# Kernel tuning notes

Measured on AMD Instinct MI355X. Metric: run time of the kernel, lower is better.

## Reference

```python
import jax, jax.numpy as jnp
import numpy as np


def setup_inputs() -> dict:
    key = jax.random.key(0)
    k1, k2, k3 = jax.random.split(key, 3)
    N = 20000
    # valid [x1, y1, x2, y2] boxes: centers in [0,1000), sizes in [1,101)
    xy = jax.random.uniform(k1, (N, 2), dtype=jnp.float32) * 1000.0
    wh = jax.random.uniform(k2, (N, 2), dtype=jnp.float32) * 100.0 + 1.0
    boxes = jnp.concatenate([xy, xy + wh], axis=1)
    scores = jax.random.uniform(k3, (N,), dtype=jnp.float32)
    return {
        "boxes": boxes,
        "scores": scores,
        "max_output_size": 1000,
        "iou_threshold": 0.5,
        "scores_threshold": 0.1,
    }


def reference(boxes, scores, max_output_size, iou_threshold, scores_threshold):
    boxes = boxes.astype(jnp.float32)
    scores = scores.astype(jnp.float32)
    N = boxes.shape[0]

    # score filtering: instead of physically filtering (dynamic shape),
    # mark below-threshold boxes as pre-suppressed and push them to the
    # end of the stable descending sort with -inf keys.
    valid = scores > scores_threshold
    sort_key = jnp.where(valid, scores, -jnp.inf)
    order = jnp.argsort(-sort_key)  # jnp.argsort is stable -> stable descending

    sboxes = boxes[order]                      # [N,4] score-sorted boxes
    svalid = valid[order]
    sorig = order.astype(jnp.int32)            # original indices, sorted
    areas = (sboxes[:, 2] - sboxes[:, 0]) * (sboxes[:, 3] - sboxes[:, 1])
    idx = jnp.arange(N)

    def body(carry, i):
        suppressed, selected, count = carry
        can = jnp.logical_and(~suppressed[i], count < max_output_size)
        selected = jnp.where(can, selected.at[count].set(sorig[i]), selected)
        # vectorized IoU of box i against all boxes (only j > i matter)
        b = sboxes[i]
        x1 = jnp.maximum(b[0], sboxes[:, 0])
        y1 = jnp.maximum(b[1], sboxes[:, 1])
        x2 = jnp.minimum(b[2], sboxes[:, 2])
        y2 = jnp.minimum(b[3], sboxes[:, 3])
        inter = jnp.maximum(x2 - x1, 0.0) * jnp.maximum(y2 - y1, 0.0)
        union = jnp.maximum(areas[i] + areas - inter, 1e-6)
        iou = inter / union
        suppressed = suppressed | (can & (idx > i) & (iou >= iou_threshold))
        count = count + can.astype(jnp.int32)
        return (suppressed, selected, count), None

    init = (~svalid, jnp.zeros(max_output_size, dtype=jnp.int32), jnp.int32(0))
    (_, selected, count), _ = jax.lax.scan(body, init, idx)
    return selected, count
```

## Files before the change

### kernel.cpp

```cpp
#include <hip/hip_runtime.h>
#include <cstdint>

typedef unsigned long long u64;

#define TOPK 2048
#define MW2 (TOPK / 64)
#define CAND 4096
#define HIST_BLOCKS 8
#define COMPACT_BLOCKS 32
#define RANK_BLOCKS (CAND / 64)
#define FB_WORDS 1024


__device__ __forceinline__ unsigned score_ud(float s, float thr) {
    unsigned u = __float_as_uint(s);
    u ^= (u >> 31) ? 0xFFFFFFFFu : 0x80000000u;
    unsigned ud = ~u;
    if (!(s > thr)) ud = 0xFFFFFFFFu;
    return ud;
}

__global__ __launch_bounds__(256) void hist_kernel(const float* __restrict__ scores,
                                                   const float* __restrict__ thrPtr,
                                                   int* __restrict__ slices,
                                                   int* __restrict__ meta, int N) {
    __shared__ int h[4096];
    int tid = threadIdx.x;
    for (int b = tid; b < 4096; b += 256) h[b] = 0;
    if (blockIdx.x == 0 && tid == 0) meta[0] = 0;
    __syncthreads();
    float thr = *thrPtr;
    for (int i = blockIdx.x * 256 + tid; i < N; i += HIST_BLOCKS * 256) {
        unsigned ud = score_ud(scores[i], thr);
        if (ud != 0xFFFFFFFFu) atomicAdd(&h[ud >> 20], 1);
    }
    __syncthreads();
    int* myslice = slices + blockIdx.x * 4096;
    for (int b = tid; b < 4096; b += 256) myslice[b] = h[b];
}

__global__ __launch_bounds__(256) void compact_kernel(
        const float* __restrict__ scores, const float* __restrict__ thrPtr,
        const int* __restrict__ slices, int* __restrict__ meta,
        u64* __restrict__ ckeys, int N, int maxNeed) {
    __shared__ int bins[4096];
    __shared__ int shC;
    int tid = threadIdx.x, lane = tid & 63;
    {
        const int4* sl = (const int4*)slices;
        int4* bo = (int4*)bins;
#pragma unroll
        for (int k = 0; k < 4; ++k) {
            int p = k * 256 + tid;
            int4 a = sl[p];
            int4 v1 = sl[1024 + p];
            int4 v2 = sl[2 * 1024 + p];
            int4 v3 = sl[3 * 1024 + p];
            int4 v4 = sl[4 * 1024 + p];
            int4 v5 = sl[5 * 1024 + p];
            int4 v6 = sl[6 * 1024 + p];
            int4 v7 = sl[7 * 1024 + p];
            a.x += v1.x + v2.x + v3.x + v4.x + v5.x + v6.x + v7.x;
            a.y += v1.y + v2.y + v3.y + v4.y + v5.y + v6.y + v7.y;
            a.z += v1.z + v2.z + v3.z + v4.z + v5.z + v6.z + v7.z;
            a.w += v1.w + v2.w + v3.w + v4.w + v5.w + v6.w + v7.w;
            bo[p] = a;
        }
    }
    __syncthreads();
    if (tid < 64) {
        int base = lane * 64;
        int sum = 0;
        for (int b = 0; b < 64; ++b) sum += bins[base + ((b + lane) & 63)];
        int incl = sum;
        for (int off = 1; off < 64; off <<= 1) {
            int o = __shfl_up(incl, off, 64);
            if (lane >= off) incl += o;
        }
        int total = __shfl(incl, 63, 64);
        int need = (maxNeed < total) ? maxNeed : total;
        u64 ok = __ballot(incl >= need);
        int L = (ok != 0ull) ? (int)__builtin_ctzll(ok) : 0;
        if (lane == L) {
            int acc = incl - sum;
            int C = base, Msel = acc;
            for (int b = 0; b < 64; ++b) {
                acc += bins[base + b];
                if (acc >= need) { C = base + b; Msel = acc; break; }
            }
            if (need <= 0) { C = -1; Msel = 0; }
            shC = C;
            if (blockIdx.x == 0) {
                meta[2] = Msel;
                meta[3] = (Msel > CAND) ? 1 : 0;
            }
        }
        if (lane == 0 && blockIdx.x == 0) meta[1] = total;
    }
    __syncthreads();
    int C = shC;
    float thr = *thrPtr;
    for (int i0 = blockIdx.x * 256; i0 < N; i0 += COMPACT_BLOCKS * 256) {
        int i = i0 + tid;
        bool sel = false;
        unsigned ud = 0;
        if (i < N) {
            ud = score_ud(scores[i], thr);
            sel = (ud != 0xFFFFFFFFu) && ((int)(ud >> 20) <= C);
        }
        u64 ball = __ballot(sel);
        if (ball) {
            int cntw = __popcll(ball);
            int base = 0;
            if (lane == 0) base = atomicAdd(&meta[0], cntw);
            base = __shfl(base, 0, 64);
            if (sel) {
                int slot = base + __popcll(ball & ((1ull << lane) - 1ull));
                if (slot < CAND) ckeys[slot] = ((u64)ud << 32) | (unsigned)i;
            }
        }
    }
}

__global__ __launch_bounds__(256) void rank_gather_kernel(
        const u64* __restrict__ ckeys, const int* __restrict__ meta,
        const float* __restrict__ boxes,
        float4* __restrict__ sboxes, int* __restrict__ sorig) {
    __shared__ u64 lk[CAND];
    __shared__ int part[4][64];
    int tid = threadIdx.x, lane = tid & 63, q = tid >> 6;
    int Msel = meta[2];
    if (Msel > CAND) Msel = CAND;
    for (int j = tid; j < Msel; j += 256) lk[j] = ckeys[j];
    __syncthreads();
    if (blockIdx.x * 64 >= Msel) return;
    int i = blockIdx.x * 64 + lane;
    u64 key = (i < Msel) ? lk[i] : ~0ull;
    int chunk = (Msel + 3) >> 2;
    int j0 = q * chunk;
    int j1 = j0 + chunk; if (j1 > Msel) j1 = Msel;
    int r = 0;
#pragma unroll 4
    for (int j = j0; j < j1; ++j) r += (lk[j] < key) ? 1 : 0;
    part[q][lane] = r;
    __syncthreads();
    if (q == 0 && i < Msel) {
        int rank = part[0][lane] + part[1][lane] + part[2][lane] + part[3][lane];
        if (rank < TOPK) {
            int idx = (int)(key & 0xFFFFFFFFu);
            sboxes[rank] = ((const float4*)boxes)[idx];
            sorig[rank] = idx;
        }
    }
}

__global__ __launch_bounds__(64) void mask2_kernel(
        const float4* __restrict__ sboxes, const float* __restrict__ iouThrPtr,
        u64* __restrict__ maskT, u64* __restrict__ diagT) {
    int wi = blockIdx.x, wj = blockIdx.y;
    if (wj < wi) return;
    __shared__ float jx1[64], jy1[64], jx2[64], jy2[64], ja[64];
    __shared__ u64 rowLDS[64];
    int t = threadIdx.x;
    int j0 = wj << 6;
    float4 jb = sboxes[j0 + t];
    jx1[t] = jb.x; jy1[t] = jb.y; jx2[t] = jb.z; jy2[t] = jb.w;
    ja[t] = (jb.z - jb.x) * (jb.w - jb.y);
    __syncthreads();
    int i = (wi << 6) + t;
    float thr = *iouThrPtr;
    float4 ib = sboxes[i];
    float ia = (ib.z - ib.x) * (ib.w - ib.y);
    u64 bits = 0;
    for (int jj = 0; jj < 64; ++jj) {
        int j = j0 + jj;
        if (j > i) {
            float xx1 = fmaxf(ib.x, jx1[jj]);
            float yy1 = fmaxf(ib.y, jy1[jj]);
            float xx2 = fminf(ib.z, jx2[jj]);
            float yy2 = fminf(ib.w, jy2[jj]);
            float ww = fmaxf(xx2 - xx1, 0.0f);
            float hh = fmaxf(yy2 - yy1, 0.0f);
            float inter = ww * hh;
            float uni = fmaxf(ia + ja[jj] - inter, 1e-6f);
            if (inter / uni >= thr) bits |= 1ull << jj;
        }
    }
    rowLDS[t] = bits;
    __syncthreads();
    u64 col = 0;
    for (int r = 0; r < 64; ++r) col |= ((rowLDS[r] >> t) & 1ull) << r;
    maskT[(size_t)(j0 + t) * MW2 + wi] = col;
    if (wi == wj) diagT[(wi << 6) + t] = col;
}

__global__ __launch_bounds__(1024) void scan2_kernel(
        const u64* __restrict__ maskT, const u64* __restrict__ diagT,
        const int* __restrict__ sorig, const int* __restrict__ meta,
        const float* __restrict__ boxes, const float* __restrict__ scores,
        const float* __restrict__ iouThrPtr, const float* __restrict__ scoreThrPtr,
        int* __restrict__ out, int N, int maxOut) {
    __shared__ u64 diagLDS[TOPK];
    __shared__ u64 selw[MW2];
    __shared__ u64 validwLDS[MW2];
    __shared__ u64 ballots[4];
    __shared__ int selLDS[TOPK];
    __shared__ int cntSh;
    __shared__ u64 aliveW[FB_WORDS];
    __shared__ u64 keyRed[16];
    __shared__ u64 winKeySh;
    int tid = threadIdx.x, lane = tid & 63, wave = tid >> 6;

    int Msel = meta[2];
    int V = (Msel < TOPK) ? Msel : TOPK;
    for (int k = tid; k < TOPK; k += 1024) diagLDS[k] = diagT[k];
    if (tid < MW2) {
        int lo = tid * 64;
        u64 vw = (V >= lo + 64) ? ~0ull : ((V > lo) ? ((1ull << (V - lo)) - 1ull) : 0ull);
        validwLDS[tid] = vw;
        selw[tid] = 0ull;
    }
    if (tid == 0) cntSh = 0;

    ulonglong2 a0, a1, a2, a3;
    int cc = tid >> 2, g = tid & 3;
    if (tid < 256) {
        const ulonglong2* p = (const ulonglong2*)(maskT + (size_t)cc * MW2 + g * 8);
        a0 = p[0]; a1 = p[1]; a2 = p[2]; a3 = p[3];
    }
    __syncthreads();

    int cnt = 0;
    for (int w = 0; w < MW2; ++w) {
        if (tid < 256) {
            u64 wd0 = a0.x, wd1 = a0.y, wd2 = a1.x, wd3 = a1.y;
            u64 wd4 = a2.x, wd5 = a2.y, wd6 = a3.x, wd7 = a3.y;
            int wr0 = g * 8;
            u64 acc = 0;
            if (wr0 + 0 < w) acc |= wd0 & selw[wr0 + 0];
            if (wr0 + 1 < w) acc |= wd1 & selw[wr0 + 1];
            if (wr0 + 2 < w) acc |= wd2 & selw[wr0 + 2];
            if (wr0 + 3 < w) acc |= wd3 & selw[wr0 + 3];
            if (wr0 + 4 < w) acc |= wd4 & selw[wr0 + 4];
            if (wr0 + 5 < w) acc |= wd5 & selw[wr0 + 5];
            if (wr0 + 6 < w) acc |= wd6 & selw[wr0 + 6];
            if (wr0 + 7 < w) acc |= wd7 & selw[wr0 + 7];
            acc |= __shfl_xor(acc, 1, 64);
            acc |= __shfl_xor(acc, 2, 64);
            u64 B = __ballot(acc != 0ull);
            if (lane == 0) ballots[wave] = B;
            if (w + 1 < MW2) {
                const ulonglong2* p = (const ulonglong2*)(maskT + (size_t)((w + 1) * 64 + cc) * MW2 + g * 8);
                a0 = p[0]; a1 = p[1]; a2 = p[2]; a3 = p[3];
            }
        }
        __syncthreads();
        if (wave == 0) {
            u64 bv = ballots[lane >> 4];
            bool crossk = (bv >> ((lane & 15) << 2)) & 1ull;
            bool alv = ((validwLDS[w] >> lane) & 1ull) && !crossk;
            u64 inm = diagLDS[(w << 6) | lane];
            u64 sel = __ballot(alv);
            for (int it = 0; it < 64; ++it) {
                bool killed = (inm & sel) != 0ull;
                u64 ns = __ballot(alv && !killed);
                if (ns == sel) break;
                sel = ns;
            }
            int room = maxOut - cnt;
            int tot = __popcll(sel);
            u64 below = (1ull << lane) - 1ull;
            if (tot > room) {
                bool keep = ((sel >> lane) & 1ull) && (__popcll(sel & below) < room);
                sel = __ballot(keep);
                tot = room;
            }
            if ((sel >> lane) & 1ull) {
                int pos = cnt + __popcll(sel & below);
                selLDS[pos] = (w << 6) | lane;
            }
            if (lane == 0) { selw[w] = sel; cntSh = cnt + tot; }
        }
        __syncthreads();
        cnt = cntSh;
        if (cnt >= maxOut) break;
    }

    int vt = meta[1];
    int f2 = meta[3];
    bool complete = (f2 == 0) && ((cnt >= maxOut) || (V >= vt));
    if (complete) {
        for (int k = tid; k < cnt; k += 1024) out[k] = sorig[selLDS[k]];
        for (int k = cnt + tid; k < maxOut; k += 1024) out[k] = 0;
        if (tid == 0) out[maxOut] = cnt;
        return;
    }

    float sThr = *scoreThrPtr, iThr = *iouThrPtr;
    for (int e0 = wave << 6; e0 < N; e0 += 1024) {
        int e = e0 + lane;
        bool a = (e < N) && (scores[e] > sThr);
        u64 ball = __ballot(a);
        if (lane == 0) aliveW[e0 >> 6] = ball;
    }
    __syncthreads();
    int fcnt = 0;
    while (fcnt < maxOut) {
        u64 best = 0;
        for (int e = tid; e < N; e += 1024) {
            if ((aliveW[e >> 6] >> (e & 63)) & 1ull) {
                float s = scores[e];
                unsigned u = __float_as_uint(s);
                u ^= (u >> 31) ? 0xFFFFFFFFu : 0x80000000u;
                u64 k = ((u64)u << 32) | (unsigned)(~e);
                if (k > best) best = k;
            }
        }
#pragma unroll
        for (int off = 32; off >= 1; off >>= 1) {
            u64 o = __shfl_xor(best, off, 64);
            if (o > best) best = o;
        }
        if (lane == 0) keyRed[wave] = best;
        __syncthreads();
        if (tid == 0) {
            u64 b = 0;
            for (int p = 0; p < 16; ++p) if (keyRed[p] > b) b = keyRed[p];
            winKeySh = b;
        }
        __syncthreads();
        u64 wk = winKeySh;
        if (wk == 0ull) break;
        int win = (int)(~(unsigned)wk);
        if (tid == 0) out[fcnt] = win;
        ++fcnt;
        float4 wb = ((const float4*)boxes)[win];
        float wa = (wb.z - wb.x) * (wb.w - wb.y);
        for (int e0 = wave << 6; e0 < N; e0 += 1024) {
            int e = e0 + lane;
            bool kill = false;
            if (e < N && ((aliveW[e0 >> 6] >> lane) & 1ull)) {
                if (e == win) kill = true;
                else {
                    float4 bb = ((const float4*)boxes)[e];
                    float xx1 = fmaxf(wb.x, bb.x), yy1 = fmaxf(wb.y, bb.y);
                    float xx2 = fminf(wb.z, bb.z), yy2 = fminf(wb.w, bb.w);
                    float inter = fmaxf(xx2 - xx1, 0.0f) * fmaxf(yy2 - yy1, 0.0f);
                    float ba = (bb.z - bb.x) * (bb.w - bb.y);
                    float uni = fmaxf(wa + ba - inter, 1e-6f);
                    kill = (inter / uni >= iThr);
                }
            }
            u64 kb = __ballot(kill);
            if (lane == 0 && kb) aliveW[e0 >> 6] &= ~kb;
        }
        __syncthreads();
    }
    for (int k = fcnt + tid; k < maxOut; k += 1024) out[k] = 0;
    if (tid == 0) out[maxOut] = fcnt;
}

extern "C" void kernel_launch(void* const* d_in, const int* in_sizes, int n_in,
                              void* d_out, int out_size, void* d_ws, size_t ws_size,
                              hipStream_t stream) {
    const float* boxes       = (const float*)d_in[0];
    const float* scores      = (const float*)d_in[1];
    const float* iouThrPtr   = (const float*)d_in[3];
    const float* scoreThrPtr = (const float*)d_in[4];

    int N = in_sizes[0] / 4;
    int maxOut = out_size - 1;

    char* ws = (char*)d_ws;
    size_t off = 0;
    auto take = [&](size_t b) { void* p = ws + off; off = (off + b + 255) & ~(size_t)255; return p; };
    int*    slices = (int*)   take((size_t)HIST_BLOCKS * 4096 * 4);
    int*    meta   = (int*)   take(256);
    u64*    ckeys  = (u64*)   take((size_t)CAND * 8);
    float4* sboxes = (float4*)take((size_t)TOPK * 16);
    int*    sorig  = (int*)   take((size_t)TOPK * 4);
    u64*    maskT  = (u64*)   take((size_t)TOPK * MW2 * 8);
    u64*    diagT  = (u64*)   take((size_t)MW2 * 64 * 8);
    (void)ws_size;

    hist_kernel<<<HIST_BLOCKS, 256, 0, stream>>>(scores, scoreThrPtr, slices, meta, N);
    compact_kernel<<<COMPACT_BLOCKS, 256, 0, stream>>>(scores, scoreThrPtr, slices, meta,
                                                       ckeys, N, TOPK);
    rank_gather_kernel<<<RANK_BLOCKS, 256, 0, stream>>>(ckeys, meta, boxes, sboxes, sorig);
    mask2_kernel<<<dim3(MW2, MW2), 64, 0, stream>>>(sboxes, iouThrPtr, maskT, diagT);
    scan2_kernel<<<1, 1024, 0, stream>>>(maskT, diagT, sorig, meta,
                                         boxes, scores, iouThrPtr, scoreThrPtr,
                                         (int*)d_out, N, maxOut);
}
```

Before: 64.54 us.

## Fuse NMS pipeline into single cooperative kernel with grid syncs

Replaces the five separate kernel launches (histogram, compaction, rank/gather, mask build, scan) with one cooperative kernel of 256 blocks that separates the phases with grid.sync(). The aim is to remove launch gaps and inter-kernel dependency stalls. The mask phase now packs four 64-wide tiles per block over only the upper-triangular tiles, and the histogram uses 16 blocks. In exchange, the final sequential scan runs on one 256-thread block instead of 1024 threads, and cooperative grid-sync costs are added.

```diff
diff --git a/kernel.cpp b/kernel.cpp
--- a/kernel.cpp
+++ b/kernel.cpp
@@ -1,14 +1,16 @@
 #include <hip/hip_runtime.h>
+#include <hip/hip_cooperative_groups.h>
 #include <cstdint>
 
+namespace cg = cooperative_groups;
 typedef unsigned long long u64;
 
 #define TOPK 2048
 #define MW2 (TOPK / 64)
 #define CAND 4096
-#define HIST_BLOCKS 8
-#define COMPACT_BLOCKS 32
-#define RANK_BLOCKS (CAND / 64)
+#define NB 256
+#define NT 256
+#define HISTB 16
 #define FB_WORDS 1024
 
 
@@ -20,92 +22,109 @@
     return ud;
 }
 
-__global__ __launch_bounds__(256) void hist_kernel(const float* __restrict__ scores,
-                                                   const float* __restrict__ thrPtr,
-                                                   int* __restrict__ slices,
-                                                   int* __restrict__ meta, int N) {
-    __shared__ int h[4096];
-    int tid = threadIdx.x;
-    for (int b = tid; b < 4096; b += 256) h[b] = 0;
-    if (blockIdx.x == 0 && tid == 0) meta[0] = 0;
-    __syncthreads();
-    float thr = *thrPtr;
-    for (int i = blockIdx.x * 256 + tid; i < N; i += HIST_BLOCKS * 256) {
-        unsigned ud = score_ud(scores[i], thr);
-        if (ud != 0xFFFFFFFFu) atomicAdd(&h[ud >> 20], 1);
-    }
-    __syncthreads();
-    int* myslice = slices + blockIdx.x * 4096;
-    for (int b = tid; b < 4096; b += 256) myslice[b] = h[b];
-}
-
-__global__ __launch_bounds__(256) void compact_kernel(
-        const float* __restrict__ scores, const float* __restrict__ thrPtr,
-        const int* __restrict__ slices, int* __restrict__ meta,
-        u64* __restrict__ ckeys, int N, int maxNeed) {
-    __shared__ int bins[4096];
-    __shared__ int shC;
-    int tid = threadIdx.x, lane = tid & 63;
-    {
-        const int4* sl = (const int4*)slices;
-        int4* bo = (int4*)bins;
+struct SMem {
+    union {
+        int bins[4096];
+        u64 lk[CAND];
+        struct {
+            float jx1[4][64], jy1[4][64], jx2[4][64], jy2[4][64], ja[4][64];
+            u64 rowLDS[4][64];
+        } mk;
+        struct {
+            u64 diagLDS[TOPK];
+            int selLDS[TOPK];
+            u64 aliveW[FB_WORDS];
+        } sc;
+    } u;
+    int part[4][64];
+    u64 selw[MW2];
+    u64 validwLDS[MW2];
+    u64 ballots[4];
+    u64 keyRed[4];
+    u64 winKeySh;
+    int cntSh;
+};
+
+__global__ __launch_bounds__(NT) void nms_all_kernel(
+        const float* __restrict__ scores, const float* __restrict__ scoreThrPtr,
+        const float* __restrict__ boxes, const float* __restrict__ iouThrPtr,
+        int* __restrict__ slices, int* __restrict__ meta,
+        u64* __restrict__ ckeys, float4* __restrict__ sboxes,
+        int* __restrict__ sorig, u64* __restrict__ maskT, u64* __restrict__ diagT,
+        int* __restrict__ out, int N, int maxOut) {
+    __shared__ SMem sm;
+    cg::grid_group grid = cg::this_grid();
+    int tid = threadIdx.x, lane = tid & 63, wave = tid >> 6;
+    int bid = blockIdx.x;
+    float sThr = *scoreThrPtr;
+
+    if (bid < HISTB) {
+        for (int b = tid; b < 4096; b += NT) sm.u.bins[b] = 0;
+        __syncthreads();
+        for (int i = bid * NT + tid; i < N; i += HISTB * NT) {
+            unsigned ud = score_ud(scores[i], sThr);
+            if (ud != 0xFFFFFFFFu) atomicAdd(&sm.u.bins[ud >> 20], 1);
+        }
+        __syncthreads();
+        int* sl = slices + bid * 4096;
+        for (int b = tid; b < 4096; b += NT) sl[b] = sm.u.bins[b];
+    }
+    if (bid == 0 && tid == 0) meta[0] = 0;
+    grid.sync();
+
+    if (bid == 0) {
+        const int4* sl4 = (const int4*)slices;
+        int4* bo = (int4*)sm.u.bins;
 #pragma unroll
         for (int k = 0; k < 4; ++k) {
-            int p = k * 256 + tid;
-            int4 a = sl[p];
-            int4 v1 = sl[1024 + p];
-            int4 v2 = sl[2 * 1024 + p];
-            int4 v3 = sl[3 * 1024 + p];
-            int4 v4 = sl[4 * 1024 + p];
-            int4 v5 = sl[5 * 1024 + p];
-            int4 v6 = sl[6 * 1024 + p];
-            int4 v7 = sl[7 * 1024 + p];
-            a.x += v1.x + v2.x + v3.x + v4.x + v5.x + v6.x + v7.x;
-            a.y += v1.y + v2.y + v3.y + v4.y + v5.y + v6.y + v7.y;
-            a.z += v1.z + v2.z + v3.z + v4.z + v5.z + v6.z + v7.z;
-            a.w += v1.w + v2.w + v3.w + v4.w + v5.w + v6.w + v7.w;
-            bo[p] = a;
-        }
-    }
-    __syncthreads();
-    if (tid < 64) {
-        int base = lane * 64;
-        int sum = 0;
-        for (int b = 0; b < 64; ++b) sum += bins[base + ((b + lane) & 63)];
-        int incl = sum;
-        for (int off = 1; off < 64; off <<= 1) {
-            int o = __shfl_up(incl, off, 64);
-            if (lane >= off) incl += o;
-        }
-        int total = __shfl(incl, 63, 64);
-        int need = (maxNeed < total) ? maxNeed : total;
-        u64 ok = __ballot(incl >= need);
-        int L = (ok != 0ull) ? (int)__builtin_ctzll(ok) : 0;
-        if (lane == L) {
-            int acc = incl - sum;
-            int C = base, Msel = acc;
-            for (int b = 0; b < 64; ++b) {
-                acc += bins[base + b];
-                if (acc >= need) { C = base + b; Msel = acc; break; }
-            }
-            if (need <= 0) { C = -1; Msel = 0; }
-            shC = C;
-            if (blockIdx.x == 0) {
+            int p = k * NT + tid;
+            int ax = 0, ay = 0, az = 0, aw = 0;
+#pragma unroll
+            for (int s = 0; s < HISTB; ++s) {
+                int4 v = sl4[s * 1024 + p];
+                ax += v.x; ay += v.y; az += v.z; aw += v.w;
+            }
+            int4 o; o.x = ax; o.y = ay; o.z = az; o.w = aw;
+            bo[p] = o;
+        }
+        __syncthreads();
+        if (tid < 64) {
+            int base = lane * 64;
+            int sum = 0;
+            for (int b = 0; b < 64; ++b) sum += sm.u.bins[base + ((b + lane) & 63)];
+            int incl = sum;
+            for (int off = 1; off < 64; off <<= 1) {
+                int o = __shfl_up(incl, off, 64);
+                if (lane >= off) incl += o;
+            }
+            int total = __shfl(incl, 63, 64);
+            int need = (TOPK < total) ? TOPK : total;
+            u64 ok = __ballot(incl >= need);
+            int L = (ok != 0ull) ? (int)__builtin_ctzll(ok) : 0;
+            if (lane == L) {
+                int acc = incl - sum;
+                int C = base, Msel = acc;
+                for (int b = 0; b < 64; ++b) {
+                    acc += sm.u.bins[base + b];
+                    if (acc >= need) { C = base + b; Msel = acc; break; }
+                }
+                if (need <= 0) { C = -1; Msel = 0; }
                 meta[2] = Msel;
                 meta[3] = (Msel > CAND) ? 1 : 0;
-            }
-        }
-        if (lane == 0 && blockIdx.x == 0) meta[1] = total;
-    }
-    __syncthreads();
-    int C = shC;
-    float thr = *thrPtr;
-    for (int i0 = blockIdx.x * 256; i0 < N; i0 += COMPACT_BLOCKS * 256) {
-        int i = i0 + tid;
+                meta[4] = C;
+            }
+            if (lane == 0) meta[1] = total;
+        }
+    }
+    grid.sync();
+
+    {
+        int C = meta[4];
+        int i = bid * NT + tid;
         bool sel = false;
         unsigned ud = 0;
         if (i < N) {
-            ud = score_ud(scores[i], thr);
+            ud = score_ud(scores[i], sThr);
             sel = (ud != 0xFFFFFFFFu) && ((int)(ud >> 20) <= C);
         }
         u64 ball = __ballot(sel);
@@ -120,111 +139,102 @@
             }
         }
     }
-}
-
-__global__ __launch_bounds__(256) void rank_gather_kernel(
-        const u64* __restrict__ ckeys, const int* __restrict__ meta,
-        const float* __restrict__ boxes,
-        float4* __restrict__ sboxes, int* __restrict__ sorig) {
-    __shared__ u64 lk[CAND];
-    __shared__ int part[4][64];
-    int tid = threadIdx.x, lane = tid & 63, q = tid >> 6;
-    int Msel = meta[2];
-    if (Msel > CAND) Msel = CAND;
-    for (int j = tid; j < Msel; j += 256) lk[j] = ckeys[j];
-    __syncthreads();
-    if (blockIdx.x * 64 >= Msel) return;
-    int i = blockIdx.x * 64 + lane;
-    u64 key = (i < Msel) ? lk[i] : ~0ull;
-    int chunk = (Msel + 3) >> 2;
-    int j0 = q * chunk;
-    int j1 = j0 + chunk; if (j1 > Msel) j1 = Msel;
-    int r = 0;
+    grid.sync();
+
+    {
+        int Msel = meta[2];
+        if (Msel > CAND) Msel = CAND;
+        if (bid * 64 < Msel) {
+            for (int j = tid; j < Msel; j += NT) sm.u.lk[j] = ckeys[j];
+            __syncthreads();
+            int q = tid >> 6;
+            int i = bid * 64 + lane;
+            u64 key = (i < Msel) ? sm.u.lk[i] : ~0ull;
+            int chunk = (Msel + 3) >> 2;
+            int j0 = q * chunk;
+            int j1 = j0 + chunk; if (j1 > Msel) j1 = Msel;
+            int r = 0;
 #pragma unroll 4
-    for (int j = j0; j < j1; ++j) r += (lk[j] < key) ? 1 : 0;
-    part[q][lane] = r;
-    __syncthreads();
-    if (q == 0 && i < Msel) {
-        int rank = part[0][lane] + part[1][lane] + part[2][lane] + part[3][lane];
-        if (rank < TOPK) {
-            int idx = (int)(key & 0xFFFFFFFFu);
-            sboxes[rank] = ((const float4*)boxes)[idx];
-            sorig[rank] = idx;
-        }
-    }
-}
-
-__global__ __launch_bounds__(64) void mask2_kernel(
-        const float4* __restrict__ sboxes, const float* __restrict__ iouThrPtr,
-        u64* __restrict__ maskT, u64* __restrict__ diagT) {
-    int wi = blockIdx.x, wj = blockIdx.y;
-    if (wj < wi) return;
-    __shared__ float jx1[64], jy1[64], jx2[64], jy2[64], ja[64];
-    __shared__ u64 rowLDS[64];
-    int t = threadIdx.x;
-    int j0 = wj << 6;
-    float4 jb = sboxes[j0 + t];
-    jx1[t] = jb.x; jy1[t] = jb.y; jx2[t] = jb.z; jy2[t] = jb.w;
-    ja[t] = (jb.z - jb.x) * (jb.w - jb.y);
-    __syncthreads();
-    int i = (wi << 6) + t;
-    float thr = *iouThrPtr;
-    float4 ib = sboxes[i];
-    float ia = (ib.z - ib.x) * (ib.w - ib.y);
-    u64 bits = 0;
-    for (int jj = 0; jj < 64; ++jj) {
-        int j = j0 + jj;
-        if (j > i) {
-            float xx1 = fmaxf(ib.x, jx1[jj]);
-            float yy1 = fmaxf(ib.y, jy1[jj]);
-            float xx2 = fminf(ib.z, jx2[jj]);
-            float yy2 = fminf(ib.w, jy2[jj]);
-            float ww = fmaxf(xx2 - xx1, 0.0f);
-            float hh = fmaxf(yy2 - yy1, 0.0f);
-            float inter = ww * hh;
-            float uni = fmaxf(ia + ja[jj] - inter, 1e-6f);
-            if (inter / uni >= thr) bits |= 1ull << jj;
-        }
-    }
-    rowLDS[t] = bits;
-    __syncthreads();
-    u64 col = 0;
-    for (int r = 0; r < 64; ++r) col |= ((rowLDS[r] >> t) & 1ull) << r;
-    maskT[(size_t)(j0 + t) * MW2 + wi] = col;
-    if (wi == wj) diagT[(wi << 6) + t] = col;
-}
-
-__global__ __launch_bounds__(1024) void scan2_kernel(
-        const u64* __restrict__ maskT, const u64* __restrict__ diagT,
-        const int* __restrict__ sorig, const int* __restrict__ meta,
-        const float* __restrict__ boxes, const float* __restrict__ scores,
-        const float* __restrict__ iouThrPtr, const float* __restrict__ scoreThrPtr,
-        int* __restrict__ out, int N, int maxOut) {
-    __shared__ u64 diagLDS[TOPK];
-    __shared__ u64 selw[MW2];
-    __shared__ u64 validwLDS[MW2];
-    __shared__ u64 ballots[4];
-    __shared__ int selLDS[TOPK];
-    __shared__ int cntSh;
-    __shared__ u64 aliveW[FB_WORDS];
-    __shared__ u64 keyRed[16];
-    __shared__ u64 winKeySh;
-    int tid = threadIdx.x, lane = tid & 63, wave = tid >> 6;
+            for (int j = j0; j < j1; ++j) r += (sm.u.lk[j] < key) ? 1 : 0;
+            sm.part[q][lane] = r;
+            __syncthreads();
+            if (q == 0 && i < Msel) {
+                int rank = sm.part[0][lane] + sm.part[1][lane] +
+                           sm.part[2][lane] + sm.part[3][lane];
+                if (rank < TOPK) {
+                    int idx = (int)(key & 0xFFFFFFFFu);
+                    sboxes[rank] = ((const float4*)boxes)[idx];
+                    sorig[rank] = idx;
+                }
+            }
+        }
+    }
+    grid.sync();
+
+    {
+        float iThr = *iouThrPtr;
+        int g = tid >> 6;
+        int t = bid * 4 + g;
+        const int ntiles = (MW2 * (MW2 + 1)) / 2;
+        bool act = (t < ntiles);
+        int wi = 0, tt = t;
+        if (act) { while (tt >= MW2 - wi) { tt -= MW2 - wi; ++wi; } }
+        int wj = wi + tt;
+        if (act) {
+            float4 jb = sboxes[(wj << 6) + lane];
+            sm.u.mk.jx1[g][lane] = jb.x; sm.u.mk.jy1[g][lane] = jb.y;
+            sm.u.mk.jx2[g][lane] = jb.z; sm.u.mk.jy2[g][lane] = jb.w;
+            sm.u.mk.ja[g][lane] = (jb.z - jb.x) * (jb.w - jb.y);
+        }
+        __syncthreads();
+        u64 bits = 0;
+        if (act) {
+            int i = (wi << 6) + lane;
+            float4 ib = sboxes[i];
+            float ia = (ib.z - ib.x) * (ib.w - ib.y);
+            int j0 = wj << 6;
+            for (int jj = 0; jj < 64; ++jj) {
+                int j = j0 + jj;
+                if (j > i) {
+                    float xx1 = fmaxf(ib.x, sm.u.mk.jx1[g][jj]);
+                    float yy1 = fmaxf(ib.y, sm.u.mk.jy1[g][jj]);
+                    float xx2 = fminf(ib.z, sm.u.mk.jx2[g][jj]);
+                    float yy2 = fminf(ib.w, sm.u.mk.jy2[g][jj]);
+                    float ww = fmaxf(xx2 - xx1, 0.0f);
+                    float hh = fmaxf(yy2 - yy1, 0.0f);
+                    float inter = ww * hh;
+                    float uni = fmaxf(ia + sm.u.mk.ja[g][jj] - inter, 1e-6f);
+                    if (inter / uni >= iThr) bits |= 1ull << jj;
+                }
+            }
+            sm.u.mk.rowLDS[g][lane] = bits;
+        }
+        __syncthreads();
+        if (act) {
+            u64 col = 0;
+            for (int r = 0; r < 64; ++r) col |= ((sm.u.mk.rowLDS[g][r] >> lane) & 1ull) << r;
+            maskT[(size_t)((wj << 6) + lane) * MW2 + wi] = col;
+            if (wi == wj) diagT[(wi << 6) + lane] = col;
+        }
+    }
+    grid.sync();
+
+    if (bid != 0) return;
 
     int Msel = meta[2];
     int V = (Msel < TOPK) ? Msel : TOPK;
-    for (int k = tid; k < TOPK; k += 1024) diagLDS[k] = diagT[k];
+    for (int k = tid; k < TOPK; k += NT) sm.u.sc.diagLDS[k] = diagT[k];
     if (tid < MW2) {
         int lo = tid * 64;
         u64 vw = (V >= lo + 64) ? ~0ull : ((V > lo) ? ((1ull << (V - lo)) - 1ull) : 0ull);
-        validwLDS[tid] = vw;
-        selw[tid] = 0ull;
-    }
-    if (tid == 0) cntSh = 0;
+        sm.validwLDS[tid] = vw;
+        sm.selw[tid] = 0ull;
+    }
+    if (tid == 0) sm.cntSh = 0;
 
     ulonglong2 a0, a1, a2, a3;
     int cc = tid >> 2, g = tid & 3;
-    if (tid < 256) {
+    {
         const ulonglong2* p = (const ulonglong2*)(maskT + (size_t)cc * MW2 + g * 8);
         a0 = p[0]; a1 = p[1]; a2 = p[2]; a3 = p[3];
     }
@@ -232,23 +242,23 @@
 
     int cnt = 0;
     for (int w = 0; w < MW2; ++w) {
-        if (tid < 256) {
+        {
             u64 wd0 = a0.x, wd1 = a0.y, wd2 = a1.x, wd3 = a1.y;
             u64 wd4 = a2.x, wd5 = a2.y, wd6 = a3.x, wd7 = a3.y;
             int wr0 = g * 8;
             u64 acc = 0;
-            if (wr0 + 0 < w) acc |= wd0 & selw[wr0 + 0];
-            if (wr0 + 1 < w) acc |= wd1 & selw[wr0 + 1];
-            if (wr0 + 2 < w) acc |= wd2 & selw[wr0 + 2];
-            if (wr0 + 3 < w) acc |= wd3 & selw[wr0 + 3];
-            if (wr0 + 4 < w) acc |= wd4 & selw[wr0 + 4];
-            if (wr0 + 5 < w) acc |= wd5 & selw[wr0 + 5];
-            if (wr0 + 6 < w) acc |= wd6 & selw[wr0 + 6];
-            if (wr0 + 7 < w) acc |= wd7 & selw[wr0 + 7];
+            if (wr0 + 0 < w) acc |= wd0 & sm.selw[wr0 + 0];
+            if (wr0 + 1 < w) acc |= wd1 & sm.selw[wr0 + 1];
+            if (wr0 + 2 < w) acc |= wd2 & sm.selw[wr0 + 2];
+            if (wr0 + 3 < w) acc |= wd3 & sm.selw[wr0 + 3];
+            if (wr0 + 4 < w) acc |= wd4 & sm.selw[wr0 + 4];
+            if (wr0 + 5 < w) acc |= wd5 & sm.selw[wr0 + 5];
+            if (wr0 + 6 < w) acc |= wd6 & sm.selw[wr0 + 6];
+            if (wr0 + 7 < w) acc |= wd7 & sm.selw[wr0 + 7];
             acc |= __shfl_xor(acc, 1, 64);
             acc |= __shfl_xor(acc, 2, 64);
             u64 B = __ballot(acc != 0ull);
-            if (lane == 0) ballots[wave] = B;
+            if (lane == 0) sm.ballots[wave] = B;
             if (w + 1 < MW2) {
                 const ulonglong2* p = (const ulonglong2*)(maskT + (size_t)((w + 1) * 64 + cc) * MW2 + g * 8);
                 a0 = p[0]; a1 = p[1]; a2 = p[2]; a3 = p[3];
@@ -256,10 +266,10 @@
         }
         __syncthreads();
         if (wave == 0) {
-            u64 bv = ballots[lane >> 4];
+            u64 bv = sm.ballots[lane >> 4];
             bool crossk = (bv >> ((lane & 15) << 2)) & 1ull;
-            bool alv = ((validwLDS[w] >> lane) & 1ull) && !crossk;
-            u64 inm = diagLDS[(w << 6) | lane];
+            bool alv = ((sm.validwLDS[w] >> lane) & 1ull) && !crossk;
+            u64 inm = sm.u.sc.diagLDS[(w << 6) | lane];
             u64 sel = __ballot(alv);
             for (int it = 0; it < 64; ++it) {
                 bool killed = (inm & sel) != 0ull;
@@ -277,12 +287,12 @@
             }
             if ((sel >> lane) & 1ull) {
                 int pos = cnt + __popcll(sel & below);
-                selLDS[pos] = (w << 6) | lane;
-            }
-            if (lane == 0) { selw[w] = sel; cntSh = cnt + tot; }
-        }
-        __syncthreads();
-        cnt = cntSh;
+                sm.u.sc.selLDS[pos] = (w << 6) | lane;
+            }
+            if (lane == 0) { sm.selw[w] = sel; sm.cntSh = cnt + tot; }
+        }
+        __syncthreads();
+        cnt = sm.cntSh;
         if (cnt >= maxOut) break;
     }
 
@@ -290,25 +300,25 @@
     int f2 = meta[3];
     bool complete = (f2 == 0) && ((cnt >= maxOut) || (V >= vt));
     if (complete) {
-        for (int k = tid; k < cnt; k += 1024) out[k] = sorig[selLDS[k]];
-        for (int k = cnt + tid; k < maxOut; k += 1024) out[k] = 0;
+        for (int k = tid; k < cnt; k += NT) out[k] = sorig[sm.u.sc.selLDS[k]];
+        for (int k = cnt + tid; k < maxOut; k += NT) out[k] = 0;
         if (tid == 0) out[maxOut] = cnt;
         return;
     }
 
-    float sThr = *scoreThrPtr, iThr = *iouThrPtr;
-    for (int e0 = wave << 6; e0 < N; e0 += 1024) {
+    float iThr = *iouThrPtr;
+    for (int e0 = wave << 6; e0 < N; e0 += NT) {
         int e = e0 + lane;
         bool a = (e < N) && (scores[e] > sThr);
         u64 ball = __ballot(a);
-        if (lane == 0) aliveW[e0 >> 6] = ball;
+        if (lane == 0) sm.u.sc.aliveW[e0 >> 6] = ball;
     }
     __syncthreads();
     int fcnt = 0;
     while (fcnt < maxOut) {
         u64 best = 0;
-        for (int e = tid; e < N; e += 1024) {
-            if ((aliveW[e >> 6] >> (e & 63)) & 1ull) {
+        for (int e = tid; e < N; e += NT) {
+            if ((sm.u.sc.aliveW[e >> 6] >> (e & 63)) & 1ull) {
                 float s = scores[e];
                 unsigned u = __float_as_uint(s);
                 u ^= (u >> 31) ? 0xFFFFFFFFu : 0x80000000u;
@@ -321,25 +331,25 @@
             u64 o = __shfl_xor(best, off, 64);
             if (o > best) best = o;
         }
-        if (lane == 0) keyRed[wave] = best;
+        if (lane == 0) sm.keyRed[wave] = best;
         __syncthreads();
         if (tid == 0) {
             u64 b = 0;
-            for (int p = 0; p < 16; ++p) if (keyRed[p] > b) b = keyRed[p];
-            winKeySh = b;
-        }
-        __syncthreads();
-        u64 wk = winKeySh;
+            for (int p = 0; p < 4; ++p) if (sm.keyRed[p] > b) b = sm.keyRed[p];
+            sm.winKeySh = b;
+        }
+        __syncthreads();
+        u64 wk = sm.winKeySh;
         if (wk == 0ull) break;
         int win = (int)(~(unsigned)wk);
         if (tid == 0) out[fcnt] = win;
         ++fcnt;
         float4 wb = ((const float4*)boxes)[win];
         float wa = (wb.z - wb.x) * (wb.w - wb.y);
-        for (int e0 = wave << 6; e0 < N; e0 += 1024) {
+        for (int e0 = wave << 6; e0 < N; e0 += NT) {
             int e = e0 + lane;
             bool kill = false;
-            if (e < N && ((aliveW[e0 >> 6] >> lane) & 1ull)) {
+            if (e < N && ((sm.u.sc.aliveW[e0 >> 6] >> lane) & 1ull)) {
                 if (e == win) kill = true;
                 else {
                     float4 bb = ((const float4*)boxes)[e];
@@ -352,11 +362,11 @@
                 }
             }
             u64 kb = __ballot(kill);
-            if (lane == 0 && kb) aliveW[e0 >> 6] &= ~kb;
-        }
-        __syncthreads();
-    }
-    for (int k = fcnt + tid; k < maxOut; k += 1024) out[k] = 0;
+            if (lane == 0 && kb) sm.u.sc.aliveW[e0 >> 6] &= ~kb;
+        }
+        __syncthreads();
+    }
+    for (int k = fcnt + tid; k < maxOut; k += NT) out[k] = 0;
     if (tid == 0) out[maxOut] = fcnt;
 }
 
@@ -374,7 +384,7 @@
     char* ws = (char*)d_ws;
     size_t off = 0;
     auto take = [&](size_t b) { void* p = ws + off; off = (off + b + 255) & ~(size_t)255; return p; };
-    int*    slices = (int*)   take((size_t)HIST_BLOCKS * 4096 * 4);
+    int*    slices = (int*)   take((size_t)HISTB * 4096 * 4);
     int*    meta   = (int*)   take(256);
     u64*    ckeys  = (u64*)   take((size_t)CAND * 8);
     float4* sboxes = (float4*)take((size_t)TOPK * 16);
@@ -382,13 +392,13 @@
     u64*    maskT  = (u64*)   take((size_t)TOPK * MW2 * 8);
     u64*    diagT  = (u64*)   take((size_t)MW2 * 64 * 8);
     (void)ws_size;
-
-    hist_kernel<<<HIST_BLOCKS, 256, 0, stream>>>(scores, scoreThrPtr, slices, meta, N);
-    compact_kernel<<<COMPACT_BLOCKS, 256, 0, stream>>>(scores, scoreThrPtr, slices, meta,
-                                                       ckeys, N, TOPK);
-    rank_gather_kernel<<<RANK_BLOCKS, 256, 0, stream>>>(ckeys, meta, boxes, sboxes, sorig);
-    mask2_kernel<<<dim3(MW2, MW2), 64, 0, stream>>>(sboxes, iouThrPtr, maskT, diagT);
-    scan2_kernel<<<1, 1024, 0, stream>>>(maskT, diagT, sorig, meta,
-                                         boxes, scores, iouThrPtr, scoreThrPtr,
-                                         (int*)d_out, N, maxOut);
+    int* outp = (int*)d_out;
+
+    void* args[] = {
+        (void*)&scores, (void*)&scoreThrPtr, (void*)&boxes, (void*)&iouThrPtr,
+        (void*)&slices, (void*)&meta, (void*)&ckeys, (void*)&sboxes,
+        (void*)&sorig, (void*)&maskT, (void*)&diagT, (void*)&outp,
+        (void*)&N, (void*)&maxOut
+    };
+    hipLaunchCooperativeKernel((void*)nms_all_kernel, dim3(NB), dim3(NT), args, 0, stream);
 }
```

Measured after the change: 180.0 us. +178.8%, slower.

## Fuse candidate compaction and rank-gather into one kernel, shrink scan block

Applied to the files above, without the earlier changes.

Merges compact_kernel and rank_gather_kernel into one selrank_kernel. Each of 64 blocks now scans all N scores and builds the full candidate list in LDS, then ranks only the candidates in its own index range and scatters their boxes. This drops a kernel launch and the global ckeys round trip, at the cost of every block redundantly scanning all scores. The scan kernel also moves from 1024 to 256 threads, which leaves the fallback loops with fewer threads.

```diff
diff --git a/kernel.cpp b/kernel.cpp
--- a/kernel.cpp
+++ b/kernel.cpp
@@ -7,9 +7,9 @@
 #define MW2 (TOPK / 64)
 #define CAND 4096
 #define HIST_BLOCKS 8
-#define COMPACT_BLOCKS 32
-#define RANK_BLOCKS (CAND / 64)
+#define SELB 64
 #define FB_WORDS 1024
+#define SCAN_NT 256
 
 
 __device__ __forceinline__ unsigned score_ud(float s, float thr) {
@@ -22,12 +22,10 @@
 
 __global__ __launch_bounds__(256) void hist_kernel(const float* __restrict__ scores,
                                                    const float* __restrict__ thrPtr,
-                                                   int* __restrict__ slices,
-                                                   int* __restrict__ meta, int N) {
+                                                   int* __restrict__ slices, int N) {
     __shared__ int h[4096];
     int tid = threadIdx.x;
     for (int b = tid; b < 4096; b += 256) h[b] = 0;
-    if (blockIdx.x == 0 && tid == 0) meta[0] = 0;
     __syncthreads();
     float thr = *thrPtr;
     for (int i = blockIdx.x * 256 + tid; i < N; i += HIST_BLOCKS * 256) {
@@ -39,16 +37,22 @@
     for (int b = tid; b < 4096; b += 256) myslice[b] = h[b];
 }
 
-__global__ __launch_bounds__(256) void compact_kernel(
+__global__ __launch_bounds__(256) void selrank_kernel(
         const float* __restrict__ scores, const float* __restrict__ thrPtr,
         const int* __restrict__ slices, int* __restrict__ meta,
-        u64* __restrict__ ckeys, int N, int maxNeed) {
-    __shared__ int bins[4096];
-    __shared__ int shC;
-    int tid = threadIdx.x, lane = tid & 63;
+        const float* __restrict__ boxes,
+        float4* __restrict__ sboxes, int* __restrict__ sorig, int N) {
+    __shared__ union {
+        int bins[4096];
+        struct { u64 list[CAND]; u64 own[320]; } c;
+    } sm;
+    __shared__ int part[4][64];
+    __shared__ int shC, ticket, ownCnt;
+    int tid = threadIdx.x, lane = tid & 63, bid = blockIdx.x;
+
     {
         const int4* sl = (const int4*)slices;
-        int4* bo = (int4*)bins;
+        int4* bo = (int4*)sm.bins;
 #pragma unroll
         for (int k = 0; k < 4; ++k) {
             int p = k * 256 + tid;
@@ -71,36 +75,40 @@
     if (tid < 64) {
         int base = lane * 64;
         int sum = 0;
-        for (int b = 0; b < 64; ++b) sum += bins[base + ((b + lane) & 63)];
+        for (int b = 0; b < 64; ++b) sum += sm.bins[base + ((b + lane) & 63)];
         int incl = sum;
         for (int off = 1; off < 64; off <<= 1) {
             int o = __shfl_up(incl, off, 64);
             if (lane >= off) incl += o;
         }
         int total = __shfl(incl, 63, 64);
-        int need = (maxNeed < total) ? maxNeed : total;
+        int need = (TOPK < total) ? TOPK : total;
         u64 ok = __ballot(incl >= need);
         int L = (ok != 0ull) ? (int)__builtin_ctzll(ok) : 0;
         if (lane == L) {
             int acc = incl - sum;
             int C = base, Msel = acc;
             for (int b = 0; b < 64; ++b) {
-                acc += bins[base + b];
+                acc += sm.bins[base + b];
                 if (acc >= need) { C = base + b; Msel = acc; break; }
             }
             if (need <= 0) { C = -1; Msel = 0; }
             shC = C;
-            if (blockIdx.x == 0) {
+            if (bid == 0) {
                 meta[2] = Msel;
                 meta[3] = (Msel > CAND) ? 1 : 0;
             }
         }
-        if (lane == 0 && blockIdx.x == 0) meta[1] = total;
-    }
-    __syncthreads();
+        if (lane == 0 && bid == 0) meta[1] = total;
+    }
+    if (tid == 0) { ticket = 0; ownCnt = 0; }
+    __syncthreads();
+
     int C = shC;
+    int lo = (int)(((long long)N * bid) / SELB);
+    int hi = (int)(((long long)N * (bid + 1)) / SELB);
     float thr = *thrPtr;
-    for (int i0 = blockIdx.x * 256; i0 < N; i0 += COMPACT_BLOCKS * 256) {
+    for (int i0 = 0; i0 < N; i0 += 256) {
         int i = i0 + tid;
         bool sel = false;
         unsigned ud = 0;
@@ -112,45 +120,51 @@
         if (ball) {
             int cntw = __popcll(ball);
             int base = 0;
-            if (lane == 0) base = atomicAdd(&meta[0], cntw);
+            if (lane == 0) base = atomicAdd(&ticket, cntw);
             base = __shfl(base, 0, 64);
             if (sel) {
                 int slot = base + __popcll(ball & ((1ull << lane) - 1ull));
-                if (slot < CAND) ckeys[slot] = ((u64)ud << 32) | (unsigned)i;
-            }
-        }
-    }
-}
-
-__global__ __launch_bounds__(256) void rank_gather_kernel(
-        const u64* __restrict__ ckeys, const int* __restrict__ meta,
-        const float* __restrict__ boxes,
-        float4* __restrict__ sboxes, int* __restrict__ sorig) {
-    __shared__ u64 lk[CAND];
-    __shared__ int part[4][64];
-    int tid = threadIdx.x, lane = tid & 63, q = tid >> 6;
-    int Msel = meta[2];
-    if (Msel > CAND) Msel = CAND;
-    for (int j = tid; j < Msel; j += 256) lk[j] = ckeys[j];
-    __syncthreads();
-    if (blockIdx.x * 64 >= Msel) return;
-    int i = blockIdx.x * 64 + lane;
-    u64 key = (i < Msel) ? lk[i] : ~0ull;
-    int chunk = (Msel + 3) >> 2;
+                if (slot < CAND) sm.c.list[slot] = ((u64)ud << 32) | (unsigned)i;
+            }
+        }
+        bool own = sel && (i >= lo) && (i < hi);
+        u64 ob = __ballot(own);
+        if (ob) {
+            int co = __popcll(ob);
+            int b2 = 0;
+            if (lane == 0) b2 = atomicAdd(&ownCnt, co);
+            b2 = __shfl(b2, 0, 64);
+            if (own) {
+                int s2 = b2 + __popcll(ob & ((1ull << lane) - 1ull));
+                if (s2 < 320) sm.c.own[s2] = ((u64)ud << 32) | (unsigned)i;
+            }
+        }
+    }
+    __syncthreads();
+
+    int M = ticket; if (M > CAND) M = CAND;
+    int oc = ownCnt; if (oc > 320) oc = 320;
+    int q = tid >> 6;
+    int chunk = (M + 3) >> 2;
     int j0 = q * chunk;
-    int j1 = j0 + chunk; if (j1 > Msel) j1 = Msel;
-    int r = 0;
+    int j1 = j0 + chunk; if (j1 > M) j1 = M;
+    for (int o0 = 0; o0 < oc; o0 += 64) {
+        int o = o0 + lane;
+        u64 key = (o < oc) ? sm.c.own[o] : ~0ull;
+        int r = 0;
 #pragma unroll 4
-    for (int j = j0; j < j1; ++j) r += (lk[j] < key) ? 1 : 0;
-    part[q][lane] = r;
-    __syncthreads();
-    if (q == 0 && i < Msel) {
-        int rank = part[0][lane] + part[1][lane] + part[2][lane] + part[3][lane];
-        if (rank < TOPK) {
-            int idx = (int)(key & 0xFFFFFFFFu);
-            sboxes[rank] = ((const float4*)boxes)[idx];
-            sorig[rank] = idx;
-        }
+        for (int j = j0; j < j1; ++j) r += (sm.c.list[j] < key) ? 1 : 0;
+        part[q][lane] = r;
+        __syncthreads();
+        if (q == 0 && o < oc) {
+            int rank = part[0][lane] + part[1][lane] + part[2][lane] + part[3][lane];
+            if (rank < TOPK) {
+                int idx = (int)(key & 0xFFFFFFFFu);
+                sboxes[rank] = ((const float4*)boxes)[idx];
+                sorig[rank] = idx;
+            }
+        }
+        __syncthreads();
     }
 }
 
@@ -194,7 +208,7 @@
     if (wi == wj) diagT[(wi << 6) + t] = col;
 }
 
-__global__ __launch_bounds__(1024) void scan2_kernel(
+__global__ __launch_bounds__(SCAN_NT) void scan2_kernel(
         const u64* __restrict__ maskT, const u64* __restrict__ diagT,
         const int* __restrict__ sorig, const int* __restrict__ meta,
         const float* __restrict__ boxes, const float* __restrict__ scores,
@@ -207,13 +221,13 @@
     __shared__ int selLDS[TOPK];
     __shared__ int cntSh;
     __shared__ u64 aliveW[FB_WORDS];
-    __shared__ u64 keyRed[16];
+    __shared__ u64 keyRed[4];
     __shared__ u64 winKeySh;
     int tid = threadIdx.x, lane = tid & 63, wave = tid >> 6;
 
     int Msel = meta[2];
     int V = (Msel < TOPK) ? Msel : TOPK;
-    for (int k = tid; k < TOPK; k += 1024) diagLDS[k] = diagT[k];
+    for (int k = tid; k < TOPK; k += SCAN_NT) diagLDS[k] = diagT[k];
     if (tid < MW2) {
         int lo = tid * 64;
         u64 vw = (V >= lo + 64) ? ~0ull : ((V > lo) ? ((1ull << (V - lo)) - 1ull) : 0ull);
@@ -224,7 +238,7 @@
 
     ulonglong2 a0, a1, a2, a3;
     int cc = tid >> 2, g = tid & 3;
-    if (tid < 256) {
+    {
         const ulonglong2* p = (const ulonglong2*)(maskT + (size_t)cc * MW2 + g * 8);
         a0 = p[0]; a1 = p[1]; a2 = p[2]; a3 = p[3];
     }
@@ -232,7 +246,7 @@
 
     int cnt = 0;
     for (int w = 0; w < MW2; ++w) {
-        if (tid < 256) {
+        {
             u64 wd0 = a0.x, wd1 = a0.y, wd2 = a1.x, wd3 = a1.y;
             u64 wd4 = a2.x, wd5 = a2.y, wd6 = a3.x, wd7 = a3.y;
             int wr0 = g * 8;
@@ -290,14 +304,14 @@
     int f2 = meta[3];
     bool complete = (f2 == 0) && ((cnt >= maxOut) || (V >= vt));
     if (complete) {
-        for (int k = tid; k < cnt; k += 1024) out[k] = sorig[selLDS[k]];
-        for (int k = cnt + tid; k < maxOut; k += 1024) out[k] = 0;
+        for (int k = tid; k < cnt; k += SCAN_NT) out[k] = sorig[selLDS[k]];
+        for (int k = cnt + tid; k < maxOut; k += SCAN_NT) out[k] = 0;
         if (tid == 0) out[maxOut] = cnt;
         return;
     }
 
     float sThr = *scoreThrPtr, iThr = *iouThrPtr;
-    for (int e0 = wave << 6; e0 < N; e0 += 1024) {
+    for (int e0 = wave << 6; e0 < N; e0 += SCAN_NT) {
         int e = e0 + lane;
         bool a = (e < N) && (scores[e] > sThr);
         u64 ball = __ballot(a);
@@ -307,7 +321,7 @@
     int fcnt = 0;
     while (fcnt < maxOut) {
         u64 best = 0;
-        for (int e = tid; e < N; e += 1024) {
+        for (int e = tid; e < N; e += SCAN_NT) {
             if ((aliveW[e >> 6] >> (e & 63)) & 1ull) {
                 float s = scores[e];
                 unsigned u = __float_as_uint(s);
@@ -325,7 +339,7 @@
         __syncthreads();
         if (tid == 0) {
             u64 b = 0;
-            for (int p = 0; p < 16; ++p) if (keyRed[p] > b) b = keyRed[p];
+            for (int p = 0; p < 4; ++p) if (keyRed[p] > b) b = keyRed[p];
             winKeySh = b;
         }
         __syncthreads();
@@ -336,7 +350,7 @@
         ++fcnt;
         float4 wb = ((const float4*)boxes)[win];
         float wa = (wb.z - wb.x) * (wb.w - wb.y);
-        for (int e0 = wave << 6; e0 < N; e0 += 1024) {
+        for (int e0 = wave << 6; e0 < N; e0 += SCAN_NT) {
             int e = e0 + lane;
             bool kill = false;
             if (e < N && ((aliveW[e0 >> 6] >> lane) & 1ull)) {
@@ -356,7 +370,7 @@
         }
         __syncthreads();
     }
-    for (int k = fcnt + tid; k < maxOut; k += 1024) out[k] = 0;
+    for (int k = fcnt + tid; k < maxOut; k += SCAN_NT) out[k] = 0;
     if (tid == 0) out[maxOut] = fcnt;
 }
 
@@ -376,19 +390,17 @@
     auto take = [&](size_t b) { void* p = ws + off; off = (off + b + 255) & ~(size_t)255; return p; };
     int*    slices = (int*)   take((size_t)HIST_BLOCKS * 4096 * 4);
     int*    meta   = (int*)   take(256);
-    u64*    ckeys  = (u64*)   take((size_t)CAND * 8);
     float4* sboxes = (float4*)take((size_t)TOPK * 16);
     int*    sorig  = (int*)   take((size_t)TOPK * 4);
     u64*    maskT  = (u64*)   take((size_t)TOPK * MW2 * 8);
     u64*    diagT  = (u64*)   take((size_t)MW2 * 64 * 8);
     (void)ws_size;
 
-    hist_kernel<<<HIST_BLOCKS, 256, 0, stream>>>(scores, scoreThrPtr, slices, meta, N);
-    compact_kernel<<<COMPACT_BLOCKS, 256, 0, stream>>>(scores, scoreThrPtr, slices, meta,
-                                                       ckeys, N, TOPK);
-    rank_gather_kernel<<<RANK_BLOCKS, 256, 0, stream>>>(ckeys, meta, boxes, sboxes, sorig);
+    hist_kernel<<<HIST_BLOCKS, 256, 0, stream>>>(scores, scoreThrPtr, slices, N);
+    selrank_kernel<<<SELB, 256, 0, stream>>>(scores, scoreThrPtr, slices, meta,
+                                             boxes, sboxes, sorig, N);
     mask2_kernel<<<dim3(MW2, MW2), 64, 0, stream>>>(sboxes, iouThrPtr, maskT, diagT);
-    scan2_kernel<<<1, 1024, 0, stream>>>(maskT, diagT, sorig, meta,
-                                         boxes, scores, iouThrPtr, scoreThrPtr,
-                                         (int*)d_out, N, maxOut);
-}
+    scan2_kernel<<<1, SCAN_NT, 0, stream>>>(maskT, diagT, sorig, meta,
+                                            boxes, scores, iouThrPtr, scoreThrPtr,
+                                            (int*)d_out, N, maxOut);
+}
```

Measured after the change: 84.79 us. 1.31x slower.
